# Kernel optimization log

Measured on AMD Instinct MI355X. Metric: run time of the kernel, lower is better.

Reference implementation:

```python
import jax, jax.numpy as jnp
import numpy as np
from jax import lax

C = 64; H = 128; W = 256; HW = H * W
HIDDEN = 64
D_STATE = 64; HEADDIM = 64; EXPAND = 2; CHUNK = 256; CONV_K = 4
D_INNER = EXPAND * C            # 128
NHEADS = D_INNER // HEADDIM     # 2
CONV_DIM = D_INNER + 2 * D_STATE  # 256
D_IN_PROJ = 2 * D_INNER + 2 * D_STATE + NHEADS  # 386
RECORD_LEN = [5, 3, 4, 2]
EPS = 1e-5


def setup_inputs() -> dict:
    key = jax.random.key(0)
    ks = jax.random.split(key, 16)
    def nrm(k, shape, scale=0.02):
        return scale * jax.random.normal(k, shape, jnp.float32)
    return {
        "xx": jax.random.normal(ks[0], (sum(RECORD_LEN), C, H, W), jnp.float32),
        "record_len": jnp.array(RECORD_LEN, jnp.int32),
        "score_w1": nrm(ks[1], (HIDDEN, C)),
        "score_b1": jnp.zeros((HIDDEN,), jnp.float32),
        "score_w2": nrm(ks[2], (1, HIDDEN)),
        "score_b2": jnp.zeros((1,), jnp.float32),
        "q_w": nrm(ks[3], (C, C)), "q_b": jnp.zeros((C,), jnp.float32),
        "k_w": nrm(ks[4], (C, C)), "k_b": jnp.zeros((C,), jnp.float32),
        "v_w": nrm(ks[5], (C, C)), "v_b": jnp.zeros((C,), jnp.float32),
        "ln_w": jnp.ones((C,), jnp.float32), "ln_b": jnp.zeros((C,), jnp.float32),
        "in_proj_w": nrm(ks[6], (D_IN_PROJ, C)),
        "in_proj_b": jnp.zeros((D_IN_PROJ,), jnp.float32),
        "conv_w": nrm(ks[7], (CONV_DIM, 1, CONV_K), 0.1),
        "conv_b": jnp.zeros((CONV_DIM,), jnp.float32),
        "dt_bias": 0.1 * jax.random.normal(ks[8], (NHEADS,), jnp.float32),
        "A_log": jnp.log(jnp.arange(1, NHEADS + 1, dtype=jnp.float32)),
        "ssd_D": jnp.ones((NHEADS,), jnp.float32),
        "rms_w": jnp.ones((D_INNER,), jnp.float32),
        "out_proj_w": nrm(ks[9], (C, D_INNER)),
    }


def _segsum(x):
    # x: (..., T) -> (..., T, T) with sum_{j<k<=i} x[k] below diagonal, -inf above
    T = x.shape[-1]
    cs = jnp.cumsum(x, -1)
    ss = cs[..., :, None] - cs[..., None, :]
    return jnp.where(jnp.tril(jnp.ones((T, T), bool)), ss, -jnp.inf)


def _ssd(x, A, Bm, Cm):
    # Mamba2 chunked SSD. x:(b,l,h,p) pre-scaled by dt; A:(b,l,h)=dt*A_head; Bm,Cm:(b,l,n) (ngroups=1)
    b, l, h, p = x.shape
    c = l // CHUNK
    x = x.reshape(b, c, CHUNK, h, p)
    A = A.reshape(b, c, CHUNK, h).transpose(0, 3, 1, 2)            # (b,h,c,cl)
    Bm = Bm.reshape(b, c, CHUNK, -1)
    Cm = Cm.reshape(b, c, CHUNK, -1)
    A_cum = jnp.cumsum(A, -1)
    Lmat = jnp.exp(_segsum(A))                                     # (b,h,c,cl,cl)
    Y_diag = jnp.einsum('bcln,bcsn,bhcls,bcshp->bclhp', Cm, Bm, Lmat, x)
    decay_states = jnp.exp(A_cum[..., -1:] - A_cum)                # (b,h,c,cl)
    states = jnp.einsum('bcln,bhcl,bclhp->bchpn', Bm, decay_states, x)
    padded = jnp.pad(A_cum[..., -1], ((0, 0), (0, 0), (1, 0)))     # (b,h,c+1)
    decay_chunk = jnp.exp(_segsum(padded))                         # (b,h,c+1,c+1)
    states_cat = jnp.concatenate([jnp.zeros_like(states[:, :1]), states], 1)
    states_in = jnp.einsum('bhzc,bchpn->bzhpn', decay_chunk, states_cat)[:, :-1]
    Y_off = jnp.einsum('bcln,bchpn,bhcl->bclhp', Cm, states_in, jnp.exp(A_cum))
    return (Y_diag + Y_off).reshape(b, l, h, p)


def _forward(xx, record_len, score_w1, score_b1, score_w2, score_b2,
             q_w, q_b, k_w, k_b, v_w, v_b, ln_w, ln_b,
             in_proj_w, in_proj_b, conv_w, conv_b,
             dt_bias, A_log, ssd_D, rms_w, out_proj_w):
    rl = [int(v) for v in np.asarray(record_len)]
    # score_mlp: 1x1 convs == per-pixel channel MLP, applied to all CAVs at once
    s = jax.nn.relu(jnp.einsum('nchw,dc->ndhw', xx, score_w1) + score_b1[None, :, None, None])
    scores = (jnp.einsum('ndhw,od->nohw', s, score_w2) + score_b2[None, :, None, None])[:, 0]  # (N,H,W)
    fused = []
    start = 0
    for n in rl:  # ragged groups (variable n_cav per sample)
        grp_sc = scores[start:start + n]
        idx = jnp.argmax(grp_sc, axis=0)  # topk k=1; softmax over singleton -> weight 1
        fused.append(jnp.take_along_axis(xx[start:start + n], idx[None, None], axis=0)[0])
        start += n
    fused = jnp.stack(fused)  # (B,C,H,W)
    Bsz = fused.shape[0]
    seq = fused.reshape(Bsz, C, HW).transpose(0, 2, 1)  # (B,L,C)
    # ScaledDotProductAttention on (HW,1,C): each position attends only to itself
    q = seq @ q_w.T + q_b
    k = seq @ k_w.T + k_b
    v = seq @ v_w.T + v_b
    score = jnp.sum(q * k, -1, keepdims=True) / np.float32(np.sqrt(C))  # (B,L,1)
    attn = jax.nn.softmax(score[..., None], axis=-1)[..., 0]            # == 1
    ctx = attn * v
    # VMAMBA2 block: pre-LayerNorm -> Mamba2 SSD -> residual
    mu = jnp.mean(ctx, -1, keepdims=True)
    var = jnp.var(ctx, -1, keepdims=True)
    u = (ctx - mu) / jnp.sqrt(var + EPS) * ln_w + ln_b
    zxbcdt = u @ in_proj_w.T + in_proj_b
    z = zxbcdt[..., :D_INNER]
    xBC = zxbcdt[..., D_INNER:D_INNER + CONV_DIM]
    dt = zxbcdt[..., D_INNER + CONV_DIM:]
    xBC = lax.conv_general_dilated(xBC.transpose(0, 2, 1), conv_w, (1,), [(CONV_K - 1, 0)],
                                   dimension_numbers=('NCH', 'OIH', 'NCH'),
                                   feature_group_count=CONV_DIM)
    xBC = jax.nn.silu(xBC + conv_b[None, :, None]).transpose(0, 2, 1)  # (B,L,CONV_DIM)
    xh = xBC[..., :D_INNER].reshape(Bsz, HW, NHEADS, HEADDIM)
    Bm = xBC[..., D_INNER:D_INNER + D_STATE]
    Cm = xBC[..., D_INNER + D_STATE:]
    dt = jax.nn.softplus(dt + dt_bias)  # (B,L,h)
    A = -jnp.exp(A_log)                 # (h,)
    y = _ssd(xh * dt[..., None], dt * A, Bm, Cm)
    y = y + ssd_D[None, None, :, None] * xh
    y = y.reshape(Bsz, HW, D_INNER)
    yz = y * jax.nn.silu(z)             # gated RMSNorm
    y = yz * lax.rsqrt(jnp.mean(yz * yz, -1, keepdims=True) + EPS) * rms_w
    h = ctx + y @ out_proj_w.T
    return h.transpose(0, 2, 1).reshape(Bsz, C, H, W)


def reference(xx, record_len, score_w1, score_b1, score_w2, score_b2,
              q_w, q_b, k_w, k_b, v_w, v_b, ln_w, ln_b,
              in_proj_w, in_proj_b, conv_w, conv_b,
              dt_bias, A_log, ssd_D, rms_w, out_proj_w):
    return _forward(xx, record_len, score_w1, score_b1, score_w2, score_b2,
                    q_w, q_b, k_w, k_b, v_w, v_b, ln_w, ln_b,
                    in_proj_w, in_proj_b, conv_w, conv_b,
                    dt_bias, A_log, ssd_D, rms_w, out_proj_w)
```

## Files before the change

### kernel.cpp

```cpp
#include <hip/hip_runtime.h>
#include <cmath>

#define HW 32768
#define NC 128
#define NH 2
#define B4 4

typedef __attribute__((ext_vector_type(8))) short bf16x8;
typedef __attribute__((ext_vector_type(4))) float f32x4;
typedef __attribute__((ext_vector_type(4))) ushort u16x4;
typedef __attribute__((ext_vector_type(8))) ushort u16x8;

__device__ __forceinline__ ushort f2b(float x) {
  union { float f; unsigned u; } v; v.f = x;
  unsigned r = v.u + 0x7FFFu + ((v.u >> 16) & 1u);
  return (ushort)(r >> 16);
}
__device__ __forceinline__ float b2f(ushort b) {
  union { unsigned u; float f; } v; v.u = ((unsigned)b) << 16;
  return v.f;
}
__device__ __forceinline__ int swz(int row, int k) { return k ^ ((row & 7) << 3); }
__device__ __forceinline__ bf16x8 ldfrag(const ushort* base, int row, int k, int stride) {
  return *(const bf16x8*)(base + row * stride + swz(row, k));
}

__global__ __launch_bounds__(256) void k_score_mfma(
    const float* __restrict__ xx, const float* __restrict__ w1,
    const float* __restrict__ b1, const float* __restrict__ w2,
    const float* __restrict__ b2, float* __restrict__ scores,
    int* __restrict__ cnt)
{
  __shared__ ushort Whi[64*64];
  __shared__ ushort Wlo[64*64];
  __shared__ ushort Xt[4][64*64];
  __shared__ float w2b1[128];
  int tid = threadIdx.x;
  if (blockIdx.x == 0 && tid == 0) cnt[0] = 0;
  for (int i = tid; i < 4096; i += 256) {
    int d = i >> 6, c = i & 63;
    float v = w1[i];
    ushort hi = f2b(v);
    int off = d*64 + swz(d, c);
    Whi[off] = hi;
    Wlo[off] = f2b(v - b2f(hi));
  }
  if (tid < 64) { w2b1[tid] = w2[tid]; w2b1[64+tid] = b1[tid]; }

  int wid = tid >> 6, lane = tid & 63;
  int n  = blockIdx.x >> 7;
  int t0 = (blockIdx.x & 127)*256 + wid*64;

  {
    const float* px = xx + (size_t)n*64*HW + t0 + lane;
    float xv[64];
    #pragma unroll
    for (int c = 0; c < 64; ++c) xv[c] = px[(size_t)c*HW];
    ushort* xh = Xt[wid];
    #pragma unroll
    for (int c8 = 0; c8 < 8; ++c8) {
      u16x8 p;
      #pragma unroll
      for (int j = 0; j < 8; ++j) p[j] = f2b(xv[c8*8 + j]);
      *(u16x8*)(xh + lane*64 + swz(lane, c8*8)) = p;
    }
  }
  __syncthreads();

  int lr = lane & 15, kb = lane >> 4;
  const ushort* xh = Xt[wid];
  f32x4 acc[4][4];
  #pragma unroll
  for (int m = 0; m < 4; ++m)
    #pragma unroll
    for (int nt = 0; nt < 4; ++nt) acc[m][nt] = (f32x4){0.f,0.f,0.f,0.f};
  #pragma unroll
  for (int k0 = 0; k0 < 64; k0 += 32) {
    bf16x8 ah[4], al[4], bx[4];
    #pragma unroll
    for (int m = 0; m < 4; ++m) {
      ah[m] = ldfrag(Whi, 16*m + lr, k0 + kb*8, 64);
      al[m] = ldfrag(Wlo, 16*m + lr, k0 + kb*8, 64);
    }
    #pragma unroll
    for (int nt = 0; nt < 4; ++nt) bx[nt] = ldfrag(xh, 16*nt + lr, k0 + kb*8, 64);
    #pragma unroll
    for (int m = 0; m < 4; ++m)
      #pragma unroll
      for (int nt = 0; nt < 4; ++nt) {
        acc[m][nt] = __builtin_amdgcn_mfma_f32_16x16x32_bf16(ah[m], bx[nt], acc[m][nt], 0, 0, 0);
        acc[m][nt] = __builtin_amdgcn_mfma_f32_16x16x32_bf16(al[m], bx[nt], acc[m][nt], 0, 0, 0);
      }
  }
  float bb2 = b2[0];
  #pragma unroll
  for (int nt = 0; nt < 4; ++nt) {
    float s = 0.f;
    #pragma unroll
    for (int m = 0; m < 4; ++m)
      #pragma unroll
      for (int r = 0; r < 4; ++r) {
        int d = 16*m + kb*4 + r;
        float h = acc[m][nt][r] + w2b1[64 + d];
        s += fmaxf(h, 0.f) * w2b1[d];
      }
    s += __shfl_xor(s, 16);
    s += __shfl_xor(s, 32);
    if (kb == 0) scores[(size_t)n*HW + t0 + 16*nt + lr] = s + bb2;
  }
}

__global__ __launch_bounds__(256) void k_argmax(
    const float* __restrict__ scores, int* __restrict__ idx,
    int* __restrict__ cnt, int* __restrict__ list)
{
  int i = blockIdx.x*256 + threadIdx.x;
  int g = i >> 15, t = i & (HW-1);
  const int gs0[4] = {0,5,8,12};
  const int gl0[4] = {5,3,4,2};
  int start = gs0[g], len = gl0[g];
  float best = scores[(size_t)start*HW + t];
  float second = -3.4e38f;
  int bi = start;
  for (int j = 1; j < len; ++j) {
    float s = scores[(size_t)(start+j)*HW + t];
    if (s > best) { second = best; best = s; bi = start + j; }
    else if (s > second) second = s;
  }
  idx[i] = bi;
  if (best - second < 5e-4f) {
    int p = atomicAdd(cnt, 1);
    list[p] = i;
  }
}

__global__ __launch_bounds__(256) void k_fix(
    const float* __restrict__ xx, const float* __restrict__ w1,
    const float* __restrict__ b1, const float* __restrict__ w2,
    const float* __restrict__ b2, const int* __restrict__ cnt,
    const int* __restrict__ list, int* __restrict__ idx)
{
  __shared__ float w1f[64*65];
  __shared__ float w2f[64], b1f[64];
  int tid = threadIdx.x;
  for (int i = tid; i < 4096; i += 256) w1f[(i >> 6)*65 + (i & 63)] = w1[i];
  if (tid < 64) { w2f[tid] = w2[tid]; b1f[tid] = b1[tid]; }
  __syncthreads();
  int n = cnt[0];
  int wid = tid >> 6, lane = tid & 63;
  int nwaves = gridDim.x * 4;
  const int gs0[4] = {0,5,8,12};
  const int gl0[4] = {5,3,4,2};
  double b2d = (double)b2[0];
  for (int e = blockIdx.x*4 + wid; e < n; e += nwaves) {
    int i = list[e];
    int g = i >> 15, t = i & (HW-1);
    int start = gs0[g], len = gl0[g];
    double best = -1e300;
    int bi = start;
    for (int j = 0; j < len; ++j) {
      double xv = (double)xx[(size_t)(start+j)*64*HW + (size_t)lane*HW + t];
      double acc = (double)b1f[lane];
      #pragma unroll
      for (int c = 0; c < 64; ++c) {
        double xc = __shfl(xv, c);
        acc += xc * (double)w1f[lane*65 + c];
      }
      double sc = (acc > 0.0 ? acc : 0.0) * (double)w2f[lane];
      #pragma unroll
      for (int m = 1; m < 64; m <<= 1) sc += __shfl_xor(sc, m);
      sc += b2d;
      if (sc > best) { best = sc; bi = start + j; }
    }
    if (lane == 0) idx[i] = bi;
  }
}

__global__ __launch_bounds__(256) void k_fuse(
    const float* __restrict__ xx, const int* __restrict__ idx,
    float* __restrict__ seq)
{
  __shared__ int idxs[64];
  __shared__ float tile[64*65];
  int tid = threadIdx.x;
  int g  = blockIdx.x >> 9;
  int t0 = (blockIdx.x & 511) << 6;
  if (tid < 64) idxs[tid] = idx[(size_t)g*HW + t0 + tid];
  __syncthreads();
  int tl = tid & 63, cq = tid >> 6;
  for (int r = 0; r < 16; ++r) {
    int c = r*4 + cq;
    tile[c*65 + tl] = xx[(size_t)idxs[tl]*64*HW + (size_t)c*HW + t0 + tl];
  }
  __syncthreads();
  for (int r = 0; r < 16; ++r) {
    int row = r*4 + cq;
    seq[((size_t)g*HW + t0 + row)*64 + tl] = tile[tl*65 + row];
  }
}

__global__ __launch_bounds__(256) void k_vln(
    const float* __restrict__ seq, const float* __restrict__ vw,
    const float* __restrict__ vb, const float* __restrict__ lnw,
    const float* __restrict__ lnb, float* __restrict__ ctx,
    ushort* __restrict__ usw)
{
  __shared__ float st[64*64];
  int tid = threadIdx.x;
  size_t p0 = (size_t)blockIdx.x * 64;
  for (int i = tid; i < 64*64; i += 256) st[i] = seq[p0*64 + i];
  int o = tid & 63, wv = tid >> 6;
  float w[64];
  const float4* w4 = (const float4*)(vw + o*64);
  #pragma unroll
  for (int c4 = 0; c4 < 16; ++c4) {
    float4 v = w4[c4];
    w[c4*4+0]=v.x; w[c4*4+1]=v.y; w[c4*4+2]=v.z; w[c4*4+3]=v.w;
  }
  float bias = vb[o], lw = lnw[o], lb = lnb[o];
  __syncthreads();
  const float4* st4 = (const float4*)st;
  for (int j = 0; j < 16; ++j) {
    int p = wv*16 + j;
    float acc = bias;
    #pragma unroll
    for (int c4 = 0; c4 < 16; ++c4) {
      float4 s4 = st4[p*16 + c4];
      acc += s4.x*w[c4*4] + s4.y*w[c4*4+1] + s4.z*w[c4*4+2] + s4.w*w[c4*4+3];
    }
    float s1 = acc, s2 = acc*acc;
    #pragma unroll
    for (int m = 1; m < 64; m <<= 1) {
      s1 += __shfl_xor(s1, m);
      s2 += __shfl_xor(s2, m);
    }
    float mu  = s1*(1.f/64.f);
    float var = s2*(1.f/64.f) - mu*mu;
    float rstd = rsqrtf(var + 1e-5f);
    size_t base = (p0+p)*64;
    int gt = (int)(p0 + p);
    ctx[base + o] = acc;
    usw[base + (o ^ (((gt+3)&7)<<3))] = f2b((acc - mu)*rstd*lw + lb);
  }
}

__global__ __launch_bounds__(256) void k_prep(
    const float* __restrict__ ipw, ushort* __restrict__ wsw)
{
  int i = blockIdx.x*256 + threadIdx.x;
  int row = i >> 6, c = i & 63;
  float v = (row < 386) ? ipw[row*64 + c] : 0.f;
  wsw[row*64 + swz(row, c)] = f2b(v);
}

__global__ __launch_bounds__(512) void k_gemm(
    const ushort* __restrict__ usw, const ushort* __restrict__ wsw,
    const float* __restrict__ ipb, const float* __restrict__ dtbias,
    ushort* __restrict__ z, ushort* __restrict__ xbcT, float* __restrict__ dt)
{
  __shared__ ushort Wlds[400*64];
  __shared__ ushort Ulds[80*64];
  __shared__ ushort trans[8704];
  int tid = threadIdx.x;
  int b  = blockIdx.x >> 9;
  int t0 = (blockIdx.x & 511) << 6;
  size_t pixbase = (size_t)b*HW + t0;

  for (int i = tid; i < 3200; i += 512)
    *(u16x8*)(Wlds + i*8) = *(const u16x8*)(wsw + i*8);
  {
    const ushort* ubase = usw + ((size_t)b*HW + t0 - 3)*64;
    for (int i = tid; i < 536; i += 512) {
      u16x8 v;
      if (t0 == 0 && i < 24) v = (u16x8){0,0,0,0,0,0,0,0};
      else v = *(const u16x8*)(ubase + i*8);
      *(u16x8*)(Ulds + i*8) = v;
    }
  }
  __syncthreads();

  int w = tid >> 6, lane = tid & 63, lr = lane & 15, kb = lane >> 4;
  for (int rd = 0; rd < 3; ++rd) {
    int nt = rd*8 + w;
    f32x4 acc[5];
    #pragma unroll
    for (int mt = 0; mt < 5; ++mt) acc[mt] = (f32x4){0.f,0.f,0.f,0.f};
    #pragma unroll
    for (int kk = 0; kk < 64; kk += 32) {
      bf16x8 bfrag = ldfrag(Wlds, nt*16 + lr, kk + kb*8, 64);
      #pragma unroll
      for (int mt = 0; mt < 5; ++mt) {
        bf16x8 afrag = ldfrag(Ulds, mt*16 + lr, kk + kb*8, 64);
        acc[mt] = __builtin_amdgcn_mfma_f32_16x16x32_bf16(afrag, bfrag, acc[mt], 0, 0, 0);
      }
    }
    float bias = ipb[nt*16 + lr];
    if (rd == 0) {
      #pragma unroll
      for (int mt = 0; mt < 5; ++mt)
        #pragma unroll
        for (int r = 0; r < 4; ++r) {
          int t = mt*16 + kb*4 + r - 3;
          if (t >= 0 && t < 64) trans[t*132 + w*16 + lr] = f2b(acc[mt][r] + bias);
        }
    } else {
      #pragma unroll
      for (int mt = 0; mt < 5; ++mt)
        #pragma unroll
        for (int r = 0; r < 4; ++r) {
          int t = mt*16 + kb*4 + r - 3;
          if (t >= 0 && t < 64) trans[(w*16 + lr)*68 + t] = f2b(acc[mt][r] + bias);
        }
    }
    __syncthreads();
    if (rd == 0) {
      for (int i = tid; i < 2048; i += 512) {
        int t = i >> 5, c4 = (i & 31)*4;
        *(u16x4*)(z + (pixbase + t)*128 + c4) = *(const u16x4*)(trans + t*132 + c4);
      }
    } else {
      int chbase = (rd - 1)*128;
      for (int i = tid; i < 2048; i += 512) {
        int ch = i >> 4, t4 = (i & 15)*4;
        *(u16x4*)(xbcT + ((size_t)b*256 + chbase + ch)*HW + t0 + t4)
            = *(const u16x4*)(trans + ch*68 + t4);
      }
    }
    __syncthreads();
  }

  if (w == 0) {
    f32x4 acc[5];
    #pragma unroll
    for (int mt = 0; mt < 5; ++mt) acc[mt] = (f32x4){0.f,0.f,0.f,0.f};
    #pragma unroll
    for (int kk = 0; kk < 64; kk += 32) {
      bf16x8 bfrag = ldfrag(Wlds, 384 + lr, kk + kb*8, 64);
      #pragma unroll
      for (int mt = 0; mt < 5; ++mt) {
        bf16x8 afrag = ldfrag(Ulds, mt*16 + lr, kk + kb*8, 64);
        acc[mt] = __builtin_amdgcn_mfma_f32_16x16x32_bf16(afrag, bfrag, acc[mt], 0, 0, 0);
      }
    }
    if (lr < 2) {
      float bias = ipb[384 + lr] + dtbias[lr];
      #pragma unroll
      for (int mt = 0; mt < 5; ++mt)
        #pragma unroll
        for (int r = 0; r < 4; ++r) {
          int t = mt*16 + kb*4 + r - 3;
          if (t >= 0 && t < 64) {
            float a = acc[mt][r] + bias;
            dt[(pixbase + t)*2 + lr] = (a > 20.f) ? a : log1pf(expf(a));
          }
        }
    }
  }
}

__global__ __launch_bounds__(256) void k_conv(
    const ushort* __restrict__ xbcT, const float* __restrict__ convw,
    const float* __restrict__ convb,
    ushort* __restrict__ xhT, ushort* __restrict__ BmT,
    ushort* __restrict__ Bm, ushort* __restrict__ Cm)
{
  __shared__ ushort bmc[64*132];
  int tid = threadIdx.x;
  int b  = blockIdx.x >> 9;
  int t0 = (blockIdx.x & 511) << 6;
  int t = tid & 63, cq = tid >> 6;
  int gt = t0 + t;
  for (int it = 0; it < 64; ++it) {
    int ch = cq*64 + it;
    const ushort* src = xbcT + ((size_t)b*256 + ch)*HW + gt;
    float in0 = (gt >= 3) ? b2f(src[-3]) : 0.f;
    float in1 = (gt >= 2) ? b2f(src[-2]) : 0.f;
    float in2 = (gt >= 1) ? b2f(src[-1]) : 0.f;
    float in3 = b2f(src[0]);
    float a = convb[ch] + convw[ch*4]*in0 + convw[ch*4+1]*in1
            + convw[ch*4+2]*in2 + convw[ch*4+3]*in3;
    float s = a / (1.f + __expf(-a));
    ushort sv = f2b(s);
    if (ch < 128) {
      xhT[((size_t)b*128 + ch)*HW + gt] = sv;
    } else if (ch < 192) {
      BmT[((size_t)b*64 + ch - 128)*HW + gt] = sv;
      bmc[t*132 + (ch - 128)] = sv;
    } else {
      bmc[t*132 + 64 + (ch - 192)] = sv;
    }
  }
  __syncthreads();
  size_t tg = (size_t)b*HW + t0;
  for (int i = tid; i < 1024; i += 256) {
    int tt = i >> 4, n4 = (i & 15)*4;
    *(u16x4*)(Bm + (tg + tt)*64 + n4) = *(const u16x4*)(bmc + tt*132 + n4);
    *(u16x4*)(Cm + (tg + tt)*64 + n4) = *(const u16x4*)(bmc + tt*132 + 64 + n4);
  }
}

__global__ __launch_bounds__(256) void k_states(
    const float* __restrict__ dt, const ushort* __restrict__ xhT,
    const ushort* __restrict__ BmT, const float* __restrict__ A_log,
    float* __restrict__ states, float* __restrict__ A_last)
{
  extern __shared__ char smem[];
  float* ac  = (float*)smem;
  float* dec = ac + 256;
  ushort* xdT = (ushort*)(dec + 256);
  ushort* BT  = xdT + 16384;
  int tid = threadIdx.x;
  int ci = blockIdx.x, h = blockIdx.y, b = blockIdx.z;
  size_t tb = (size_t)ci*256;
  size_t tg = (size_t)b*HW + tb;
  float Aneg = -expf(A_log[h]);
  float dv = dt[(tg + tid)*2 + h];
  ac[tid] = dv*Aneg;
  __syncthreads();
  for (int off = 1; off < 256; off <<= 1) {
    float v = (tid >= off) ? ac[tid - off] : 0.f;
    __syncthreads();
    ac[tid] += v;
    __syncthreads();
  }
  float alast = ac[255];
  dec[tid] = dv * __expf(alast - ac[tid]);
  __syncthreads();
  for (int i = tid; i < 64*32; i += 256) {
    int p = i >> 5, lc = (i & 31) * 8;
    u16x8 xv = *(const u16x8*)(xhT + ((size_t)b*128 + h*64 + p)*HW + tb + lc);
    u16x8 o;
    #pragma unroll
    for (int e = 0; e < 8; ++e) o[e] = f2b(b2f(xv[e]) * dec[lc + e]);
    *(u16x8*)(xdT + p*256 + swz(p, lc)) = o;
    u16x8 bv = *(const u16x8*)(BmT + ((size_t)b*64 + p)*HW + tb + lc);
    *(u16x8*)(BT + p*256 + swz(p, lc)) = bv;
  }
  __syncthreads();
  int w = tid >> 6, lane = tid & 63, lr = lane & 15, kb = lane >> 4;
  f32x4 acc[4];
  #pragma unroll
  for (int m = 0; m < 4; ++m) acc[m] = (f32x4){0.f,0.f,0.f,0.f};
  for (int k0 = 0; k0 < 256; k0 += 32) {
    bf16x8 bfrag = ldfrag(BT, 16*w + lr, k0 + kb*8, 256);
    #pragma unroll
    for (int m = 0; m < 4; ++m) {
      bf16x8 afrag = ldfrag(xdT, 16*m + lr, k0 + kb*8, 256);
      acc[m] = __builtin_amdgcn_mfma_f32_16x16x32_bf16(afrag, bfrag, acc[m], 0, 0, 0);
    }
  }
  size_t sb = (((size_t)b*NC + ci)*NH + h)*4096;
  #pragma unroll
  for (int m = 0; m < 4; ++m)
    #pragma unroll
    for (int r = 0; r < 4; ++r)
      states[sb + (size_t)(16*m + kb*4 + r)*64 + 16*w + lr] = acc[m][r];
  if (tid == 0) A_last[((size_t)b*NH + h)*NC + ci] = alast;
}

__global__ __launch_bounds__(256) void k_scan(
    const float* __restrict__ states, const float* __restrict__ A_last,
    float* __restrict__ states_in)
{
  __shared__ float ef[NC];
  int tid = threadIdx.x;
  int seg = blockIdx.x & 7, h = (blockIdx.x >> 3) & 1, b = blockIdx.x >> 4;
  if (tid < NC) ef[tid] = __expf(A_last[((size_t)b*NH + h)*NC + tid]);
  __syncthreads();
  size_t base0 = (((size_t)b*NC)*NH + h)*4096 + seg*512 + tid;
  const size_t cstride = (size_t)NH*4096;
  float s0 = 0.f, s1 = 0.f;
  float ld0 = states[base0], ld1 = states[base0 + 256];
  for (int zc = 0; zc < NC; ++zc) {
    size_t cur = base0 + (size_t)zc*cstride;
    float n0 = 0.f, n1 = 0.f;
    if (zc < NC-1) { n0 = states[cur + cstride]; n1 = states[cur + cstride + 256]; }
    states_in[cur] = s0; states_in[cur + 256] = s1;
    float e = ef[zc];
    s0 = ld0 + e*s0; s1 = ld1 + e*s1;
    ld0 = n0; ld1 = n1;
  }
}

__global__ __launch_bounds__(512) void k_ydiag(
    const float* __restrict__ dt, const ushort* __restrict__ xhT,
    const ushort* __restrict__ Bm, const ushort* __restrict__ Cm,
    const float* __restrict__ states_in, const float* __restrict__ A_log,
    const float* __restrict__ ssd_D, ushort* __restrict__ y)
{
  extern __shared__ char smem[];
  float* ac   = (float*)smem;
  float* dts  = ac + 256;
  float* segs = dts + 256;
  ushort* Cb  = (ushort*)(segs + 8);
  ushort* Bb  = Cb + 16384;
  ushort* xsT = Bb + 16384;
  ushort* Sb  = xsT + 16384;
  ushort* Wb  = Sb + 4096;
  int tid = threadIdx.x;
  int ci = blockIdx.x, h = blockIdx.y, b = blockIdx.z;
  size_t tb = (size_t)ci*256;
  size_t tg = (size_t)b*HW + tb;
  int w = tid >> 6, lane = tid & 63, lr = lane & 15, kb = lane >> 4;
  float Aneg = -expf(A_log[h]);

  float dv = 0.f, a = 0.f;
  if (tid < 256) {
    dv = dt[(tg + tid)*2 + h];
    a = dv*Aneg;
    #pragma unroll
    for (int d = 1; d < 64; d <<= 1) {
      float t = __shfl_up(a, d);
      if (lane >= d) a += t;
    }
    if (lane == 63) segs[w] = a;
  }
  __syncthreads();
  if (tid < 256) {
    float off = 0.f;
    #pragma unroll
    for (int j = 0; j < 4; ++j) if (j < w) off += segs[j];
    ac[tid] = a + off;
    dts[tid] = dv;
  }
  __syncthreads();

  for (int i = tid; i < 256*16; i += 512) {
    int l = i >> 4, n4 = (i & 15) * 4;
    u16x4 cv = *(const u16x4*)(Cm + (tg + l)*64 + n4);
    *(u16x4*)(Cb + l*64 + swz(l, n4)) = cv;
    u16x4 bv = *(const u16x4*)(Bm + (tg + l)*64 + n4);
    *(u16x4*)(Bb + l*64 + swz(l, n4)) = bv;
  }
  for (int i = tid; i < 64*32; i += 512) {
    int p = i >> 5, sc = (i & 31) * 8;
    u16x8 xv = *(const u16x8*)(xhT + ((size_t)b*128 + h*64 + p)*HW + tb + sc);
    u16x8 o;
    #pragma unroll
    for (int e = 0; e < 8; ++e) o[e] = f2b(b2f(xv[e]) * dts[sc + e]);
    *(u16x8*)(xsT + p*256 + swz(p, sc)) = o;
  }
  size_t sbg = (((size_t)b*NC + ci)*NH + h)*4096;
  for (int i = tid; i < 1024; i += 512) {
    int p = i >> 4, n4 = (i & 15) * 4;
    float4 sv = *(const float4*)(states_in + sbg + p*64 + n4);
    u16x4 pk = { f2b(sv.x), f2b(sv.y), f2b(sv.z), f2b(sv.w) };
    *(u16x4*)(Sb + p*64 + swz(p, n4)) = pk;
  }
  __syncthreads();

  int l0 = w*32;
  ushort* Ww = Wb + w*2048;

  f32x4 yy[2][4];
  #pragma unroll
  for (int m = 0; m < 2; ++m)
    #pragma unroll
    for (int n = 0; n < 4; ++n) yy[m][n] = (f32x4){0.f,0.f,0.f,0.f};
  #pragma unroll
  for (int kk = 0; kk < 64; kk += 32) {
    bf16x8 af[2], bf[4];
    #pragma unroll
    for (int m = 0; m < 2; ++m) af[m] = ldfrag(Cb, l0 + 16*m + lr, kk + kb*8, 64);
    #pragma unroll
    for (int n = 0; n < 4; ++n) bf[n] = ldfrag(Sb, 16*n + lr, kk + kb*8, 64);
    #pragma unroll
    for (int m = 0; m < 2; ++m)
      #pragma unroll
      for (int n = 0; n < 4; ++n)
        yy[m][n] = __builtin_amdgcn_mfma_f32_16x16x32_bf16(af[m], bf[n], yy[m][n], 0, 0, 0);
  }
  #pragma unroll
  for (int m = 0; m < 2; ++m)
    #pragma unroll
    for (int r = 0; r < 4; ++r) {
      float e = __expf(ac[l0 + 16*m + kb*4 + r]);
      #pragma unroll
      for (int n = 0; n < 4; ++n) yy[m][n][r] *= e;
    }

  int nst = (w >> 1) + 1;
  for (int st = 0; st < nst; ++st) {
    int s0 = st*64;
    f32x4 g[2][4];
    #pragma unroll
    for (int m = 0; m < 2; ++m)
      #pragma unroll
      for (int n = 0; n < 4; ++n) g[m][n] = (f32x4){0.f,0.f,0.f,0.f};
    #pragma unroll
    for (int kk = 0; kk < 64; kk += 32) {
      bf16x8 af[2], bf[4];
      #pragma unroll
      for (int m = 0; m < 2; ++m) af[m] = ldfrag(Cb, l0 + 16*m + lr, kk + kb*8, 64);
      #pragma unroll
      for (int n = 0; n < 4; ++n) bf[n] = ldfrag(Bb, s0 + 16*n + lr, kk + kb*8, 64);
      #pragma unroll
      for (int m = 0; m < 2; ++m)
        #pragma unroll
        for (int n = 0; n < 4; ++n)
          g[m][n] = __builtin_amdgcn_mfma_f32_16x16x32_bf16(af[m], bf[n], g[m][n], 0, 0, 0);
    }
    #pragma unroll
    for (int m = 0; m < 2; ++m)
      #pragma unroll
      for (int r = 0; r < 4; ++r) {
        int lrow = 16*m + kb*4 + r;
        int lg = l0 + lrow;
        float acl = ac[lg];
        #pragma unroll
        for (int n = 0; n < 4; ++n) {
          int sl = 16*n + lr;
          int sg = s0 + sl;
          float v = (sg <= lg) ? g[m][n][r] * __expf(acl - ac[sg]) : 0.f;
          Ww[lrow*64 + swz(lrow, sl)] = f2b(v);
        }
      }
    #pragma unroll
    for (int kk = 0; kk < 64; kk += 32) {
      bf16x8 af[2], bf[4];
      #pragma unroll
      for (int m = 0; m < 2; ++m) af[m] = ldfrag(Ww, 16*m + lr, kk + kb*8, 64);
      #pragma unroll
      for (int n = 0; n < 4; ++n) bf[n] = ldfrag(xsT, 16*n + lr, s0 + kk + kb*8, 256);
      #pragma unroll
      for (int m = 0; m < 2; ++m)
        #pragma unroll
        for (int n = 0; n < 4; ++n)
          yy[m][n] = __builtin_amdgcn_mfma_f32_16x16x32_bf16(af[m], bf[n], yy[m][n], 0, 0, 0);
    }
  }

  float Dh = ssd_D[h];
  #pragma unroll
  for (int m = 0; m < 2; ++m)
    #pragma unroll
    for (int r = 0; r < 4; ++r) {
      int lg = l0 + 16*m + kb*4 + r;
      float f = Dh / dts[lg];
      #pragma unroll
      for (int n = 0; n < 4; ++n) {
        int p = 16*n + lr;
        float val = yy[m][n][r] + f * b2f(xsT[p*256 + swz(p, lg)]);
        y[(tg + lg)*128 + h*64 + p] = f2b(val);
      }
    }
}

__global__ __launch_bounds__(256) void k_final(
    const ushort* __restrict__ y, const ushort* __restrict__ z,
    const float* __restrict__ ctx, const float* __restrict__ rms_w,
    const float* __restrict__ opw, float* __restrict__ out)
{
  __shared__ ushort yn[64*128];
  __shared__ ushort wop[64*128];
  __shared__ float otile[64*65];
  int tid = threadIdx.x;
  size_t p0 = (size_t)blockIdx.x * 64;

  for (int i = tid; i < 2048; i += 256) {
    int row = i >> 5, c4 = (i & 31) * 4;
    float4 v = ((const float4*)(opw + row*128))[c4 >> 2];
    float4 rw = ((const float4*)rms_w)[c4 >> 2];
    u16x4 p = { f2b(v.x*rw.x), f2b(v.y*rw.y), f2b(v.z*rw.z), f2b(v.w*rw.w) };
    *(u16x4*)(wop + row*128 + swz(row, c4)) = p;
  }

  {
    int t = tid >> 2, q = tid & 3;
    const u16x4* yp = (const u16x4*)(y + (p0 + t)*128 + q*32);
    const u16x4* zp = (const u16x4*)(z + (p0 + t)*128 + q*32);
    float vals[32];
    float ss = 0.f;
    #pragma unroll
    for (int j = 0; j < 8; ++j) {
      u16x4 yv = yp[j];
      u16x4 zv = zp[j];
      #pragma unroll
      for (int e = 0; e < 4; ++e) {
        float zf = b2f(zv[e]);
        float x = b2f(yv[e]) * (zf / (1.f + __expf(-zf)));
        vals[j*4+e] = x; ss += x*x;
      }
    }
    ss += __shfl_xor(ss, 1);
    ss += __shfl_xor(ss, 2);
    float rinv = rsqrtf(ss*(1.f/128.f) + 1e-5f);
    #pragma unroll
    for (int j = 0; j < 8; ++j) {
      int c4 = q*32 + j*4;
      u16x4 p = { f2b(vals[j*4]*rinv), f2b(vals[j*4+1]*rinv),
                  f2b(vals[j*4+2]*rinv), f2b(vals[j*4+3]*rinv) };
      *(u16x4*)(yn + t*128 + swz(t, c4)) = p;
    }
  }
  __syncthreads();

  int w = tid >> 6, lane = tid & 63, lr = lane & 15, kb = lane >> 4;
  f32x4 acc[4];
  #pragma unroll
  for (int n = 0; n < 4; ++n) acc[n] = (f32x4){0.f,0.f,0.f,0.f};
  #pragma unroll
  for (int kk = 0; kk < 128; kk += 32) {
    bf16x8 a = ldfrag(yn, w*16 + lr, kk + kb*8, 128);
    #pragma unroll
    for (int n = 0; n < 4; ++n) {
      bf16x8 bf = ldfrag(wop, n*16 + lr, kk + kb*8, 128);
      acc[n] = __builtin_amdgcn_mfma_f32_16x16x32_bf16(a, bf, acc[n], 0, 0, 0);
    }
  }
  #pragma unroll
  for (int n = 0; n < 4; ++n)
    #pragma unroll
    for (int r = 0; r < 4; ++r) {
      int tok = w*16 + kb*4 + r, ch = n*16 + lr;
      otile[ch*65 + tok] = acc[n][r] + ctx[(p0 + tok)*64 + ch];
    }
  __syncthreads();
  {
    size_t b  = p0 >> 15;
    size_t t0 = p0 & (HW-1);
    for (int r = 0; r < 16; ++r) {
      int cc = r*4 + (tid >> 6);
      int pp = tid & 63;
      out[(b*64 + cc)*HW + t0 + pp] = otile[cc*65 + pp];
    }
  }
}

extern "C" void kernel_launch(void* const* d_in, const int* in_sizes, int n_in,
                              void* d_out, int out_size, void* d_ws, size_t ws_size,
                              hipStream_t stream) {
  (void)in_sizes; (void)n_in; (void)out_size; (void)ws_size;
  const float* xx   = (const float*)d_in[0];
  const float* sw1  = (const float*)d_in[2];
  const float* sb1  = (const float*)d_in[3];
  const float* sw2  = (const float*)d_in[4];
  const float* sb2  = (const float*)d_in[5];
  const float* vw   = (const float*)d_in[10];
  const float* vb   = (const float*)d_in[11];
  const float* lnw  = (const float*)d_in[12];
  const float* lnb  = (const float*)d_in[13];
  const float* ipw  = (const float*)d_in[14];
  const float* ipb  = (const float*)d_in[15];
  const float* cw   = (const float*)d_in[16];
  const float* cb   = (const float*)d_in[17];
  const float* dtb  = (const float*)d_in[18];
  const float* alog = (const float*)d_in[19];
  const float* sd   = (const float*)d_in[20];
  const float* rmsw = (const float*)d_in[21];
  const float* opw  = (const float*)d_in[22];

  float* ws = (float*)d_ws;
  float*  scores32 = ws;
  int*    idxb     = (int*)(ws + 458752);
  int*    cntb     = (int*)(ws + 589824);
  int*    listb    = (int*)(ws + 589832);
  float*  dtp      = ws;
  float*  seq      = ws + 917504;
  ushort* Cmb      = (ushort*)(ws + 917504);
  ushort* BmTb     = (ushort*)(ws + 5111808);
  float*  ctx      = ws + 9306112;
  ushort* uswb     = (ushort*)(ws + 17694720);
  float*  states   = ws + 17694720;
  float*  states_in= ws + 21889024;
  ushort* zb       = (ushort*)(ws + 26083328);
  ushort* xbcTb    = (ushort*)(ws + 34471936);
  ushort* xhTb     = (ushort*)(ws + 51249152);
  ushort* Bmb      = (ushort*)(ws + 59637760);
  ushort* yb       = (ushort*)(ws + 68026368);
  float*  Alast    = ws + 84803584;
  ushort* wswb     = (ushort*)(ws + 84804608);

  k_score_mfma<<<1792, 256, 0, stream>>>(xx, sw1, sb1, sw2, sb2, scores32, cntb);
  k_argmax<<<512, 256, 0, stream>>>(scores32, idxb, cntb, listb);
  k_fix<<<512, 256, 0, stream>>>(xx, sw1, sb1, sw2, sb2, cntb, listb, idxb);
  k_fuse<<<2048, 256, 0, stream>>>(xx, idxb, seq);
  k_vln<<<2048, 256, 0, stream>>>(seq, vw, vb, lnw, lnb, ctx, uswb);
  k_prep<<<100, 256, 0, stream>>>(ipw, wswb);
  k_gemm<<<2048, 512, 0, stream>>>(uswb, wswb, ipb, dtb, zb, xbcTb, dtp);
  k_conv<<<2048, 256, 0, stream>>>(xbcTb, cw, cb, xhTb, BmTb, Bmb, Cmb);
  dim3 gssd(NC, NH, B4);
  k_states<<<gssd, 256, 67584, stream>>>(dtp, xhTb, BmTb, alog, states, Alast);
  k_scan<<<64, 256, 0, stream>>>(states, Alast, states_in);
  k_ydiag<<<gssd, 512, 141344, stream>>>(dtp, xhTb, Bmb, Cmb, states_in, alog, sd, yb);
  k_final<<<2048, 256, 0, stream>>>(yb, zb, ctx, rmsw, opw, (float*)d_out);
}
```

Measured before the change: 463.1 us.

## Store conv inputs/outputs in per-tile blocked layout and vectorize depthwise conv

The GEMM now writes the xBC channels in a tiled layout (each 64-pixel tile holds all 256 channels contiguously) instead of channel-major rows spanning the full sequence. The conv kernel reads 8 consecutive pixels per lane with vector loads, gets halo values via lane shuffles or a small read from the previous tile, and writes one combined blocked output. That output replaces the separate xhT and BmT buffers and is read by k_states and k_ydiag. The aim is fewer scalar strided global accesses and fewer separate write streams in conv, in exchange for more complex indexing and a swizzled LDS transpose for the Bm/Cm output.

```diff
diff --git a/kernel.cpp b/kernel.cpp
--- a/kernel.cpp
+++ b/kernel.cpp
@@ -256,15 +256,17 @@
 __global__ __launch_bounds__(512) void k_gemm(
     const ushort* __restrict__ usw, const ushort* __restrict__ wsw,
     const float* __restrict__ ipb, const float* __restrict__ dtbias,
-    ushort* __restrict__ z, ushort* __restrict__ xbcT, float* __restrict__ dt)
+    ushort* __restrict__ z, ushort* __restrict__ xbcB, float* __restrict__ dt)
 {
   __shared__ ushort Wlds[400*64];
   __shared__ ushort Ulds[80*64];
   __shared__ ushort trans[8704];
   int tid = threadIdx.x;
   int b  = blockIdx.x >> 9;
-  int t0 = (blockIdx.x & 511) << 6;
+  int s  = blockIdx.x & 511;
+  int t0 = s << 6;
   size_t pixbase = (size_t)b*HW + t0;
+  size_t tilebase = ((size_t)(b*512 + s))*256*64;
 
   for (int i = tid; i < 3200; i += 512)
     *(u16x8*)(Wlds + i*8) = *(const u16x8*)(wsw + i*8);
@@ -322,7 +324,7 @@
       int chbase = (rd - 1)*128;
       for (int i = tid; i < 2048; i += 512) {
         int ch = i >> 4, t4 = (i & 15)*4;
-        *(u16x4*)(xbcT + ((size_t)b*256 + chbase + ch)*HW + t0 + t4)
+        *(u16x4*)(xbcB + tilebase + (size_t)(chbase + ch)*64 + t4)
             = *(const u16x4*)(trans + ch*68 + t4);
       }
     }
@@ -359,49 +361,77 @@
 }
 
 __global__ __launch_bounds__(256) void k_conv(
-    const ushort* __restrict__ xbcT, const float* __restrict__ convw,
-    const float* __restrict__ convb,
-    ushort* __restrict__ xhT, ushort* __restrict__ BmT,
+    const ushort* __restrict__ xbcB, const float* __restrict__ convw,
+    const float* __restrict__ convb, ushort* __restrict__ co2,
     ushort* __restrict__ Bm, ushort* __restrict__ Cm)
 {
   __shared__ ushort bmc[64*132];
   int tid = threadIdx.x;
   int b  = blockIdx.x >> 9;
-  int t0 = (blockIdx.x & 511) << 6;
-  int t = tid & 63, cq = tid >> 6;
-  int gt = t0 + t;
-  for (int it = 0; it < 64; ++it) {
-    int ch = cq*64 + it;
-    const ushort* src = xbcT + ((size_t)b*256 + ch)*HW + gt;
-    float in0 = (gt >= 3) ? b2f(src[-3]) : 0.f;
-    float in1 = (gt >= 2) ? b2f(src[-2]) : 0.f;
-    float in2 = (gt >= 1) ? b2f(src[-1]) : 0.f;
-    float in3 = b2f(src[0]);
-    float a = convb[ch] + convw[ch*4]*in0 + convw[ch*4+1]*in1
-            + convw[ch*4+2]*in2 + convw[ch*4+3]*in3;
-    float s = a / (1.f + __expf(-a));
-    ushort sv = f2b(s);
-    if (ch < 128) {
-      xhT[((size_t)b*128 + ch)*HW + gt] = sv;
-    } else if (ch < 192) {
-      BmT[((size_t)b*64 + ch - 128)*HW + gt] = sv;
-      bmc[t*132 + (ch - 128)] = sv;
-    } else {
-      bmc[t*132 + 64 + (ch - 192)] = sv;
-    }
-  }
-  __syncthreads();
-  size_t tg = (size_t)b*HW + t0;
+  int s  = blockIdx.x & 511;
+  int lane = tid & 63, wv = tid >> 6;
+  int toct = lane & 7, chi = lane >> 3;
+  size_t tilebase = ((size_t)(b*512 + s))*256*64;
+  const ushort* tsrc = xbcB + tilebase;
+  const ushort* psrc = xbcB + tilebase - 256*64;
+
+  for (int it = 0; it < 8; ++it) {
+    int ch = wv*64 + it*8 + chi;
+    u16x8 v = *(const u16x8*)(tsrc + ch*64 + toct*8);
+    float x0 = b2f(v[0]), x1 = b2f(v[1]), x2 = b2f(v[2]), x3 = b2f(v[3]);
+    float x4 = b2f(v[4]), x5 = b2f(v[5]), x6 = b2f(v[6]), x7 = b2f(v[7]);
+    float pm1 = __shfl(x7, lane - 1);
+    float pm2 = __shfl(x6, lane - 1);
+    float pm3 = __shfl(x5, lane - 1);
+    if (toct == 0) {
+      if (s > 0) {
+        u16x4 hq = *(const u16x4*)(psrc + ch*64 + 60);
+        pm3 = b2f(hq[1]); pm2 = b2f(hq[2]); pm1 = b2f(hq[3]);
+      } else {
+        pm1 = pm2 = pm3 = 0.f;
+      }
+    }
+    float4 cw = ((const float4*)convw)[ch];
+    float cb = convb[ch];
+    float o0 = cb + cw.x*pm3 + cw.y*pm2 + cw.z*pm1 + cw.w*x0;
+    float o1 = cb + cw.x*pm2 + cw.y*pm1 + cw.z*x0  + cw.w*x1;
+    float o2 = cb + cw.x*pm1 + cw.y*x0  + cw.z*x1  + cw.w*x2;
+    float o3 = cb + cw.x*x0  + cw.y*x1  + cw.z*x2  + cw.w*x3;
+    float o4 = cb + cw.x*x1  + cw.y*x2  + cw.z*x3  + cw.w*x4;
+    float o5 = cb + cw.x*x2  + cw.y*x3  + cw.z*x4  + cw.w*x5;
+    float o6 = cb + cw.x*x3  + cw.y*x4  + cw.z*x5  + cw.w*x6;
+    float o7 = cb + cw.x*x4  + cw.y*x5  + cw.z*x6  + cw.w*x7;
+    u16x8 ov;
+    ov[0] = f2b(o0 / (1.f + __expf(-o0)));
+    ov[1] = f2b(o1 / (1.f + __expf(-o1)));
+    ov[2] = f2b(o2 / (1.f + __expf(-o2)));
+    ov[3] = f2b(o3 / (1.f + __expf(-o3)));
+    ov[4] = f2b(o4 / (1.f + __expf(-o4)));
+    ov[5] = f2b(o5 / (1.f + __expf(-o5)));
+    ov[6] = f2b(o6 / (1.f + __expf(-o6)));
+    ov[7] = f2b(o7 / (1.f + __expf(-o7)));
+    *(u16x8*)(co2 + tilebase + (size_t)ch*64 + toct*8) = ov;
+    if (ch >= 128) {
+      int c = ch - 128;
+      int csw = c ^ (toct << 2);
+      #pragma unroll
+      for (int j = 0; j < 8; ++j)
+        bmc[(toct*8 + j)*132 + csw] = ov[j];
+    }
+  }
+  __syncthreads();
+  size_t tg = (size_t)b*HW + s*64;
   for (int i = tid; i < 1024; i += 256) {
     int tt = i >> 4, n4 = (i & 15)*4;
-    *(u16x4*)(Bm + (tg + tt)*64 + n4) = *(const u16x4*)(bmc + tt*132 + n4);
-    *(u16x4*)(Cm + (tg + tt)*64 + n4) = *(const u16x4*)(bmc + tt*132 + 64 + n4);
+    int sw = (tt >> 3) << 2;
+    *(u16x4*)(Bm + (tg + tt)*64 + n4) = *(const u16x4*)(bmc + tt*132 + (n4 ^ sw));
+    *(u16x4*)(Cm + (tg + tt)*64 + n4) = *(const u16x4*)(bmc + tt*132 + ((64 + n4) ^ sw));
   }
 }
 
 __global__ __launch_bounds__(256) void k_states(
-    const float* __restrict__ dt, const ushort* __restrict__ xhT,
-    const ushort* __restrict__ BmT, const float* __restrict__ A_log,
+    const float* __restrict__ dt, const ushort* __restrict__ co2,
+    const float* __restrict__ A_log,
     float* __restrict__ states, float* __restrict__ A_last)
 {
   extern __shared__ char smem[];
@@ -411,8 +441,7 @@
   ushort* BT  = xdT + 16384;
   int tid = threadIdx.x;
   int ci = blockIdx.x, h = blockIdx.y, b = blockIdx.z;
-  size_t tb = (size_t)ci*256;
-  size_t tg = (size_t)b*HW + tb;
+  size_t tg = (size_t)b*HW + (size_t)ci*256;
   float Aneg = -expf(A_log[h]);
   float dv = dt[(tg + tid)*2 + h];
   ac[tid] = dv*Aneg;
@@ -428,12 +457,14 @@
   __syncthreads();
   for (int i = tid; i < 64*32; i += 256) {
     int p = i >> 5, lc = (i & 31) * 8;
-    u16x8 xv = *(const u16x8*)(xhT + ((size_t)b*128 + h*64 + p)*HW + tb + lc);
+    int s = (ci << 2) + (lc >> 6);
+    const ushort* cb2 = co2 + ((size_t)(b*512 + s))*256*64 + (lc & 63);
+    u16x8 xv = *(const u16x8*)(cb2 + (size_t)(h*64 + p)*64);
     u16x8 o;
     #pragma unroll
     for (int e = 0; e < 8; ++e) o[e] = f2b(b2f(xv[e]) * dec[lc + e]);
     *(u16x8*)(xdT + p*256 + swz(p, lc)) = o;
-    u16x8 bv = *(const u16x8*)(BmT + ((size_t)b*64 + p)*HW + tb + lc);
+    u16x8 bv = *(const u16x8*)(cb2 + (size_t)(128 + p)*64);
     *(u16x8*)(BT + p*256 + swz(p, lc)) = bv;
   }
   __syncthreads();
@@ -483,7 +514,7 @@
 }
 
 __global__ __launch_bounds__(512) void k_ydiag(
-    const float* __restrict__ dt, const ushort* __restrict__ xhT,
+    const float* __restrict__ dt, const ushort* __restrict__ co2,
     const ushort* __restrict__ Bm, const ushort* __restrict__ Cm,
     const float* __restrict__ states_in, const float* __restrict__ A_log,
     const float* __restrict__ ssd_D, ushort* __restrict__ y)
@@ -499,8 +530,7 @@
   ushort* Wb  = Sb + 4096;
   int tid = threadIdx.x;
   int ci = blockIdx.x, h = blockIdx.y, b = blockIdx.z;
-  size_t tb = (size_t)ci*256;
-  size_t tg = (size_t)b*HW + tb;
+  size_t tg = (size_t)b*HW + (size_t)ci*256;
   int w = tid >> 6, lane = tid & 63, lr = lane & 15, kb = lane >> 4;
   float Aneg = -expf(A_log[h]);
 
@@ -534,7 +564,8 @@
   }
   for (int i = tid; i < 64*32; i += 512) {
     int p = i >> 5, sc = (i & 31) * 8;
-    u16x8 xv = *(const u16x8*)(xhT + ((size_t)b*128 + h*64 + p)*HW + tb + sc);
+    int s = (ci << 2) + (sc >> 6);
+    u16x8 xv = *(const u16x8*)(co2 + ((size_t)(b*512 + s)*256 + h*64 + p)*64 + (sc & 63));
     u16x8 o;
     #pragma unroll
     for (int e = 0; e < 8; ++e) o[e] = f2b(b2f(xv[e]) * dts[sc + e]);
@@ -758,15 +789,14 @@
   float*  dtp      = ws;
   float*  seq      = ws + 917504;
   ushort* Cmb      = (ushort*)(ws + 917504);
-  ushort* BmTb     = (ushort*)(ws + 5111808);
+  ushort* Bmb      = (ushort*)(ws + 5111808);
   float*  ctx      = ws + 9306112;
   ushort* uswb     = (ushort*)(ws + 17694720);
   float*  states   = ws + 17694720;
   float*  states_in= ws + 21889024;
   ushort* zb       = (ushort*)(ws + 26083328);
-  ushort* xbcTb    = (ushort*)(ws + 34471936);
-  ushort* xhTb     = (ushort*)(ws + 51249152);
-  ushort* Bmb      = (ushort*)(ws + 59637760);
+  ushort* xbcBb    = (ushort*)(ws + 34471936);
+  ushort* co2b     = (ushort*)(ws + 51249152);
   ushort* yb       = (ushort*)(ws + 68026368);
   float*  Alast    = ws + 84803584;
   ushort* wswb     = (ushort*)(ws + 84804608);
@@ -777,11 +807,11 @@
   k_fuse<<<2048, 256, 0, stream>>>(xx, idxb, seq);
   k_vln<<<2048, 256, 0, stream>>>(seq, vw, vb, lnw, lnb, ctx, uswb);
   k_prep<<<100, 256, 0, stream>>>(ipw, wswb);
-  k_gemm<<<2048, 512, 0, stream>>>(uswb, wswb, ipb, dtb, zb, xbcTb, dtp);
-  k_conv<<<2048, 256, 0, stream>>>(xbcTb, cw, cb, xhTb, BmTb, Bmb, Cmb);
+  k_gemm<<<2048, 512, 0, stream>>>(uswb, wswb, ipb, dtb, zb, xbcBb, dtp);
+  k_conv<<<2048, 256, 0, stream>>>(xbcBb, cw, cb, co2b, Bmb, Cmb);
   dim3 gssd(NC, NH, B4);
-  k_states<<<gssd, 256, 67584, stream>>>(dtp, xhTb, BmTb, alog, states, Alast);
+  k_states<<<gssd, 256, 67584, stream>>>(dtp, co2b, alog, states, Alast);
   k_scan<<<64, 256, 0, stream>>>(states, Alast, states_in);
-  k_ydiag<<<gssd, 512, 141344, stream>>>(dtp, xhTb, Bmb, Cmb, states_in, alog, sd, yb);
+  k_ydiag<<<gssd, 512, 141344, stream>>>(dtp, co2b, Bmb, Cmb, states_in, alog, sd, yb);
   k_final<<<2048, 256, 0, stream>>>(yb, zb, ctx, rmsw, opw, (float*)d_out);
 }
```

Result: faster. 419.1 us (-9.5%).
